# Optimization experiments

Measured on AMD Instinct MI355X. Metric: run time of the kernel, lower is better.

## Reference

```python
import jax, jax.numpy as jnp
import numpy as np

SPATIAL_SHAPES = [(128, 128), (64, 64), (32, 32), (16, 16)]
D_MODEL = 256
N_HEADS = 8
N_LEVELS = 4
N_POINTS = 4
HEAD_DIM = D_MODEL // N_HEADS
B = 2
LEN_Q = sum(h * w for h, w in SPATIAL_SHAPES)  # 21760
LEN_IN = LEN_Q


def setup_inputs() -> dict:
    key = jax.random.key(0)
    ks = jax.random.split(key, 11)
    s = 1.0 / np.sqrt(D_MODEL).astype(np.float32)
    query = jax.random.normal(ks[0], (B, LEN_Q, D_MODEL), jnp.float32)
    reference_points = jax.random.uniform(ks[1], (B, LEN_Q, N_LEVELS, 2), jnp.float32)
    input_flatten = jax.random.normal(ks[2], (B, LEN_IN, D_MODEL), jnp.float32)
    W_off = jax.random.normal(ks[3], (D_MODEL, N_HEADS * N_LEVELS * N_POINTS * 2), jnp.float32) * s
    b_off = jnp.zeros((N_HEADS * N_LEVELS * N_POINTS * 2,), jnp.float32)
    W_attn = jax.random.normal(ks[4], (D_MODEL, N_HEADS * N_LEVELS * N_POINTS), jnp.float32) * s
    b_attn = jnp.zeros((N_HEADS * N_LEVELS * N_POINTS,), jnp.float32)
    W_val = jax.random.normal(ks[5], (D_MODEL, D_MODEL), jnp.float32) * s
    b_val = jnp.zeros((D_MODEL,), jnp.float32)
    W_out = jax.random.normal(ks[6], (D_MODEL, D_MODEL), jnp.float32) * s
    b_out = jnp.zeros((D_MODEL,), jnp.float32)
    return {"query": query, "reference_points": reference_points, "input_flatten": input_flatten,
            "W_off": W_off, "b_off": b_off, "W_attn": W_attn, "b_attn": b_attn,
            "W_val": W_val, "b_val": b_val, "W_out": W_out, "b_out": b_out}


def _ms_deform_core(value, sampling_locations, attention_weights):
    # value: (B, H, Dh, N_total); sampling_locations: (B, Lq, H, L, P, 2) in [0,1]
    # attention_weights: (B, Lq, H, L*P)
    Bv, Hn, Dh, _ = value.shape
    Lq = sampling_locations.shape[1]
    P = sampling_locations.shape[4]
    BN = Bv * Hn
    grids = 2.0 * sampling_locations - 1.0
    splits = np.cumsum([h * w for h, w in SPATIAL_SHAPES])[:-1].tolist()
    value_list = jnp.split(value, splits, axis=3)
    sampled_levels = []
    for lid, (Hh, Ww) in enumerate(SPATIAL_SHAPES):
        # (BN, H*W, Dh)
        val_flat = jnp.transpose(value_list[lid].reshape(BN, Dh, Hh * Ww), (0, 2, 1))
        # (BN, Lq, P, 2)
        g = jnp.transpose(grids[:, :, :, lid, :, :], (0, 2, 1, 3, 4)).reshape(BN, Lq, P, 2)
        ix = ((g[..., 0] + 1.0) * Ww - 1.0) / 2.0
        iy = ((g[..., 1] + 1.0) * Hh - 1.0) / 2.0
        ix0 = jnp.floor(ix).astype(jnp.int32)
        iy0 = jnp.floor(iy).astype(jnp.int32)
        ix1 = ix0 + 1
        iy1 = iy0 + 1
        fx = (ix - ix0.astype(ix.dtype))[..., None]
        fy = (iy - iy0.astype(iy.dtype))[..., None]

        def valid(yy, xx):
            return ((xx >= 0) & (xx < Ww) & (yy >= 0) & (yy < Hh)).astype(val_flat.dtype)[..., None]

        def gather(yy, xx):
            idx = (jnp.clip(yy, 0, Hh - 1) * Ww + jnp.clip(xx, 0, Ww - 1)).reshape(BN, Lq * P)
            out = jnp.take_along_axis(val_flat, idx[:, :, None], axis=1)
            return out.reshape(BN, Lq, P, Dh)

        v00 = gather(iy0, ix0) * valid(iy0, ix0)
        v01 = gather(iy0, ix1) * valid(iy0, ix1)
        v10 = gather(iy1, ix0) * valid(iy1, ix0)
        v11 = gather(iy1, ix1) * valid(iy1, ix1)
        sampled = ((1 - fx) * (1 - fy) * v00 + fx * (1 - fy) * v01
                   + (1 - fx) * fy * v10 + fx * fy * v11)  # (BN, Lq, P, Dh)
        sampled_levels.append(jnp.transpose(sampled, (0, 3, 1, 2)))  # (BN, Dh, Lq, P)
    # (BN, Dh, Lq, L*P)
    sv = jnp.stack(sampled_levels, axis=-2).reshape(BN, Dh, Lq, N_LEVELS * P)
    attn = jnp.transpose(attention_weights, (0, 2, 1, 3)).reshape(BN, 1, Lq, N_LEVELS * P)
    out = jnp.sum(sv * attn, axis=-1)  # (BN, Dh, Lq)
    out = out.reshape(Bv, Hn * Dh, Lq)
    return jnp.transpose(out, (0, 2, 1))  # (B, Lq, d_model)


def reference(query, reference_points, input_flatten, W_off, b_off, W_attn, b_attn, W_val, b_val, W_out, b_out):
    Bq, Lq, _ = query.shape
    Len_in = input_flatten.shape[1]
    value = input_flatten @ W_val + b_val  # (B, Len_in, d_model)
    offsets = (query @ W_off + b_off).reshape(Bq, Lq, N_HEADS, N_LEVELS, N_POINTS, 2)
    attn = jax.nn.softmax((query @ W_attn + b_attn).reshape(Bq, Lq, N_HEADS, N_LEVELS * N_POINTS), axis=-1)
    # normalizer is (W, H) per level
    offset_normalizer = jnp.asarray([[w, h] for h, w in SPATIAL_SHAPES], dtype=query.dtype)
    sampling_locations = (reference_points[:, :, None, :, None, :]
                          + offsets / offset_normalizer[None, None, None, :, None, :])
    value = jnp.transpose(value, (0, 2, 1)).reshape(Bq, N_HEADS, HEAD_DIM, Len_in)
    out = _ms_deform_core(value, sampling_locations, attn)
    return out @ W_out + b_out
```

## Files before the change

### kernel.cpp

```cpp
#include <hip/hip_runtime.h>
#include <hip/hip_bf16.h>
#include <type_traits>

#define B_    2
#define LQ_   21760
#define LEN_  21760
#define DM    256
#define NH    8
#define NL    4
#define NP    4
#define HD    32

#define WS_VAL   0u
#define WS_QBF   22282240u
#define WS_INBF  44564480u
#define WS_OA    66846720u
#define WS_WT    133693440u

typedef __attribute__((ext_vector_type(4))) float f32x4;
typedef __attribute__((ext_vector_type(8))) short bf16x8;
typedef __attribute__((ext_vector_type(4))) unsigned int u32x4;

__device__ __forceinline__ unsigned short f2bf(float v) {
    __hip_bfloat16 h = __float2bfloat16(v);
    return *reinterpret_cast<unsigned short*>(&h);
}
__device__ __forceinline__ unsigned int pk2bf(float a, float b) {
    return (unsigned int)f2bf(a) | ((unsigned int)f2bf(b) << 16);
}

__global__ __launch_bounds__(256) void cvt_bf16(const float* __restrict__ x,
                                                unsigned short* __restrict__ y, int n4) {
    int i = blockIdx.x * 256 + threadIdx.x;
    if (i < n4) {
        f32x4 v = __builtin_nontemporal_load((const f32x4*)x + i);
        ushort4 u;
        u.x = f2bf(v.x); u.y = f2bf(v.y); u.z = f2bf(v.z); u.w = f2bf(v.w);
        ((ushort4*)y)[i] = u;
    }
}

__global__ __launch_bounds__(256) void wt_cvt(const float* __restrict__ W,
                                              unsigned short* __restrict__ Wt,
                                              int K, int N) {
    __shared__ float tile[16][17];
    const int n0 = blockIdx.x * 16, k0 = blockIdx.y * 16;
    const int tx = threadIdx.x & 15, ty = threadIdx.x >> 4;
    tile[ty][tx] = W[(size_t)(k0 + ty) * N + n0 + tx];
    __syncthreads();
    Wt[(size_t)(n0 + ty) * K + k0 + tx] = f2bf(tile[tx][ty]);
}

template <typename TOut>
__global__ __launch_bounds__(256) void gemm_mfma(const unsigned short* __restrict__ A,
                                                 const unsigned short* __restrict__ Bt,
                                                 const float* __restrict__ bias,
                                                 const float* __restrict__ bias2,
                                                 int nsplit,
                                                 TOut* __restrict__ C,
                                                 int M, int N, int K) {
    __shared__ unsigned short As[128 * 32];
    __shared__ unsigned short Bs[128 * 32];
    const int t = threadIdx.x;
    const int wv = t >> 6;
    const int ln = t & 63;
    const int m0 = blockIdx.x * 128;
    const int n0 = blockIdx.y * 128;
    const int wm = (wv & 1) * 64;
    const int wn = (wv >> 1) * 64;
    const int lrow = ln & 15;
    const int kq = ln >> 4;

    f32x4 acc[4][4] = {};

    for (int k0 = 0; k0 < K; k0 += 32) {
#pragma unroll
        for (int c = 0; c < 2; ++c) {
            const int o = c * 4096 + wv * 1024 + ln * 16;
            const int row = o >> 6;
            const int ke = (o & 63) >> 1;
            const unsigned short* ga = A + (size_t)(m0 + row) * K + k0 + ke;
            const unsigned short* gb = Bt + (size_t)(n0 + row) * K + k0 + ke;
            __builtin_amdgcn_global_load_lds(
                (const __attribute__((address_space(1))) void*)ga,
                (__attribute__((address_space(3))) void*)((char*)As + o), 16, 0, 0);
            __builtin_amdgcn_global_load_lds(
                (const __attribute__((address_space(1))) void*)gb,
                (__attribute__((address_space(3))) void*)((char*)Bs + o), 16, 0, 0);
        }
        __syncthreads();

        bf16x8 af[4], bfr[4];
#pragma unroll
        for (int i = 0; i < 4; ++i) {
            af[i]  = *(const bf16x8*)((char*)As + (wm + i * 16 + lrow) * 64 + kq * 16);
            bfr[i] = *(const bf16x8*)((char*)Bs + (wn + i * 16 + lrow) * 64 + kq * 16);
        }
#pragma unroll
        for (int i = 0; i < 4; ++i)
#pragma unroll
            for (int j = 0; j < 4; ++j)
                acc[i][j] = __builtin_amdgcn_mfma_f32_16x16x32_bf16(af[i], bfr[j], acc[i][j], 0, 0, 0);
        __syncthreads();
    }

#pragma unroll
    for (int j = 0; j < 4; ++j) {
        const int n = n0 + wn + j * 16 + lrow;
        const float bb = (n < nsplit) ? bias[n] : bias2[n - nsplit];
#pragma unroll
        for (int i = 0; i < 4; ++i) {
            const int mrow = m0 + wm + i * 16 + kq * 4;
#pragma unroll
            for (int r = 0; r < 4; ++r) {
                const float v = acc[i][j][r] + bb;
                if constexpr (std::is_same<TOut, float>::value) {
                    C[(size_t)(mrow + r) * N + n] = v;
                } else {
                    C[(size_t)(mrow + r) * N + n] = f2bf(v);
                }
            }
        }
    }
}

#define QB 8
__global__ __launch_bounds__(256) void msda_sample3(const unsigned short* __restrict__ value,
                                                    const float* __restrict__ oa,
                                                    const float* __restrict__ refp,
                                                    unsigned short* __restrict__ samp) {
    __shared__ char smem[16384 + 256];
    unsigned int* s_pk   = (unsigned int*)smem;
    float* s_off   = (float*)smem;
    float* s_logit = (float*)(smem + 8192);
    float* s_aw    = (float*)(smem + 12288);
    float* s_ref   = (float*)(smem + 16384);

    const int t = threadIdx.x;
    const int j = blockIdx.x;
    const int bq0 = ((j & 7) * 680 + (j >> 3)) * QB;
    const int b = bq0 / LQ_;

    {
        const float* oab = oa + (size_t)bq0 * 384;
#pragma unroll
        for (int r = 0; r < 2; ++r) {
            const int i = t + r * 256;
            const int ql = i >> 6, c = i & 63;
            ((f32x4*)s_off)[ql * 64 + c] =
                __builtin_nontemporal_load((const f32x4*)(oab + (size_t)ql * 384) + c);
        }
        {
            const int ql = t >> 5, c = t & 31;
            ((f32x4*)s_logit)[ql * 32 + c] =
                __builtin_nontemporal_load((const f32x4*)(oab + (size_t)ql * 384 + 256) + c);
        }
        if (t < 16)
            ((f32x4*)s_ref)[t] = __builtin_nontemporal_load((const f32x4*)(refp + (size_t)bq0 * 8) + t);
    }
    __syncthreads();

    if (t < 64) {
        const float* lg = s_logit + (t >> 3) * 128 + (t & 7) * 16;
        float m = -1e30f;
#pragma unroll
        for (int i = 0; i < 16; ++i) m = fmaxf(m, lg[i]);
        float e[16], s = 0.f;
#pragma unroll
        for (int i = 0; i < 16; ++i) { e[i] = __expf(lg[i] - m); s += e[i]; }
        const float inv = 1.f / s;
#pragma unroll
        for (int i = 0; i < 16; ++i) s_aw[t * 16 + i] = e[i] * inv;
    }
    __syncthreads();

    unsigned int pk0[4], pk1[4], pk2[4], pk3[4];
    {
        const int Wls[4] = {128, 64, 32, 16};
        const int Hls[4] = {128, 64, 32, 16};
        const int st_[4] = {0, 16384, 20480, 21504};
#pragma unroll
        for (int ii = 0; ii < 4; ++ii) {
            const int s = t * 4 + ii;
            const int q = s >> 7;
            const int rest = s & 127;
            const int h = rest >> 4;
            const int l = (rest >> 2) & 3;
            const int Wl = Wls[l], Hl = Hls[l], base = st_[l];
            const float ix = s_ref[q * 8 + l * 2]     * (float)Wl - 0.5f + s_off[q * 256 + rest * 2];
            const float iy = s_ref[q * 8 + l * 2 + 1] * (float)Hl - 0.5f + s_off[q * 256 + rest * 2 + 1];
            const float fix = floorf(ix), fiy = floorf(iy);
            const int x0 = (int)fix, y0 = (int)fiy;
            const int x1 = x0 + 1, y1 = y0 + 1;
            const float fx = ix - fix, fy = iy - fiy;
            const bool vx0 = (x0 >= 0) & (x0 < Wl);
            const bool vx1 = (x1 >= 0) & (x1 < Wl);
            const bool vy0 = (y0 >= 0) & (y0 < Hl);
            const bool vy1 = (y1 >= 0) & (y1 < Hl);
            const int cx0 = min(max(x0, 0), Wl - 1);
            const int cx1 = min(max(x1, 0), Wl - 1);
            const int cy0 = min(max(y0, 0), Hl - 1);
            const int cy1 = min(max(y1, 0), Hl - 1);
            const float aw = s_aw[(q * 8 + h) * 16 + (rest & 15)];
            const float w00 = aw * (1.f - fx) * (1.f - fy) * (float)(vx0 && vy0);
            const float w01 = aw * fx * (1.f - fy)         * (float)(vx1 && vy0);
            const float w10 = aw * (1.f - fx) * fy         * (float)(vx0 && vy1);
            const float w11 = aw * fx * fy                 * (float)(vx1 && vy1);
            pk0[ii] = (unsigned int)(base + cy0 * Wl + cx0) | ((unsigned int)(base + cy0 * Wl + cx1) << 16);
            pk1[ii] = (unsigned int)(base + cy1 * Wl + cx0) | ((unsigned int)(base + cy1 * Wl + cx1) << 16);
            pk2[ii] = pk2bf(w00, w01);
            pk3[ii] = pk2bf(w10, w11);
        }
    }
    __syncthreads();

#pragma unroll
    for (int ii = 0; ii < 4; ++ii) {
        const int s = t * 4 + ii;
        const int q = s >> 7;
        const int h = (s >> 4) & 7;
        const int swz = ((h & 3) << 2) ^ ((((h >> 2) ^ (q & 1)) & 1) << 4);
        *(uint4*)&s_pk[(s * 4) ^ swz] = make_uint4(pk0[ii], pk1[ii], pk2[ii], pk3[ii]);
    }
    __syncthreads();

    const int q = t >> 5;
    const int w = t & 31;
    const int h = w >> 2;
    const int dg = w & 3;
    const int swz = ((h & 3) << 2) ^ ((((h >> 2) ^ (q & 1)) & 1) << 4);
    const unsigned short* vbase = value + (size_t)b * LEN_ * DM + h * HD + dg * 8;

    float acc[8] = {0.f, 0.f, 0.f, 0.f, 0.f, 0.f, 0.f, 0.f};
    const int sbase = q * 128 + h * 16;
#pragma unroll
    for (int lp = 0; lp < 16; ++lp) {
        const uint4 pk = *(const uint4*)&s_pk[((sbase + lp) * 4) ^ swz];
        const uint4 v00 = *(const uint4*)(vbase + (size_t)(pk.x & 0xffffu) * DM);
        const uint4 v01 = *(const uint4*)(vbase + (size_t)(pk.x >> 16) * DM);
        const uint4 v10 = *(const uint4*)(vbase + (size_t)(pk.y & 0xffffu) * DM);
        const uint4 v11 = *(const uint4*)(vbase + (size_t)(pk.y >> 16) * DM);
        const float w00 = __uint_as_float(pk.z << 16);
        const float w01 = __uint_as_float(pk.z & 0xffff0000u);
        const float w10 = __uint_as_float(pk.w << 16);
        const float w11 = __uint_as_float(pk.w & 0xffff0000u);
#pragma unroll
        for (int c = 0; c < 4; ++c) {
            const unsigned int u00 = (&v00.x)[c], u01 = (&v01.x)[c];
            const unsigned int u10 = (&v10.x)[c], u11 = (&v11.x)[c];
            float a0 = acc[c * 2], a1 = acc[c * 2 + 1];
            a0 = fmaf(w00, __uint_as_float(u00 << 16), a0);
            a1 = fmaf(w00, __uint_as_float(u00 & 0xffff0000u), a1);
            a0 = fmaf(w01, __uint_as_float(u01 << 16), a0);
            a1 = fmaf(w01, __uint_as_float(u01 & 0xffff0000u), a1);
            a0 = fmaf(w10, __uint_as_float(u10 << 16), a0);
            a1 = fmaf(w10, __uint_as_float(u10 & 0xffff0000u), a1);
            a0 = fmaf(w11, __uint_as_float(u11 << 16), a0);
            a1 = fmaf(w11, __uint_as_float(u11 & 0xffff0000u), a1);
            acc[c * 2] = a0;
            acc[c * 2 + 1] = a1;
        }
    }
    u32x4 o;
    o.x = pk2bf(acc[0], acc[1]);
    o.y = pk2bf(acc[2], acc[3]);
    o.z = pk2bf(acc[4], acc[5]);
    o.w = pk2bf(acc[6], acc[7]);
    __builtin_nontemporal_store(o, (u32x4*)(samp + (size_t)(bq0 + q) * 256 + h * HD + dg * 8));
}

extern "C" void kernel_launch(void* const* d_in, const int* in_sizes, int n_in,
                              void* d_out, int out_size, void* d_ws, size_t ws_size,
                              hipStream_t stream) {
    const float* query  = (const float*)d_in[0];
    const float* refp   = (const float*)d_in[1];
    const float* inpf   = (const float*)d_in[2];
    const float* W_off  = (const float*)d_in[3];
    const float* b_off  = (const float*)d_in[4];
    const float* W_attn = (const float*)d_in[5];
    const float* b_attn = (const float*)d_in[6];
    const float* W_val  = (const float*)d_in[7];
    const float* b_val  = (const float*)d_in[8];
    const float* W_out  = (const float*)d_in[9];
    const float* b_out  = (const float*)d_in[10];
    float* out = (float*)d_out;

    char* ws = (char*)d_ws;
    unsigned short* val_bf  = (unsigned short*)(ws + WS_VAL);
    unsigned short* q_bf    = (unsigned short*)(ws + WS_QBF);
    unsigned short* in_bf   = (unsigned short*)(ws + WS_INBF);
    unsigned short* samp_bf = (unsigned short*)(ws + WS_INBF);
    float* oa = (float*)(ws + WS_OA);
    unsigned short* Wt_val = (unsigned short*)(ws + WS_WT);
    unsigned short* Wt_oa  = (unsigned short*)(ws + WS_WT + 131072);
    unsigned short* Wt_out = (unsigned short*)(ws + WS_WT + 327680);

    const int M = B_ * LQ_;
    const int n4 = M * DM / 4;

    cvt_bf16<<<dim3((n4 + 255) / 256), 256, 0, stream>>>(inpf, in_bf, n4);
    cvt_bf16<<<dim3((n4 + 255) / 256), 256, 0, stream>>>(query, q_bf, n4);
    wt_cvt<<<dim3(16, 16), 256, 0, stream>>>(W_val, Wt_val, 256, 256);
    wt_cvt<<<dim3(16, 16), 256, 0, stream>>>(W_off, Wt_oa, 256, 256);
    wt_cvt<<<dim3(8, 16), 256, 0, stream>>>(W_attn, Wt_oa + 256 * 256, 256, 128);
    wt_cvt<<<dim3(16, 16), 256, 0, stream>>>(W_out, Wt_out, 256, 256);

    gemm_mfma<unsigned short><<<dim3(M / 128, 2), 256, 0, stream>>>(
        in_bf, Wt_val, b_val, b_val, 256, val_bf, M, 256, 256);
    gemm_mfma<float><<<dim3(M / 128, 3), 256, 0, stream>>>(
        q_bf, Wt_oa, b_off, b_attn, 256, oa, M, 384, 256);

    msda_sample3<<<dim3(M / QB), 256, 0, stream>>>(val_bf, oa, refp, samp_bf);

    gemm_mfma<float><<<dim3(M / 128, 2), 256, 0, stream>>>(
        samp_bf, Wt_out, b_out, b_out, 256, out, M, 256, 256);
}
```

Baseline: 328.1 us.

## Fuse fp32-to-bf16 input conversion into GEMMs and store intermediates as fp16

Drops the standalone bf16 conversion kernels for query and input. The value and offset/attention GEMMs now read fp32 rows directly, convert them in registers and write bf16 into shared memory. The value and offset/logit intermediates are stored as fp16 instead of bf16/fp32 to cut the sampler's traffic. The four weight-transpose launches are merged into one, and the sampling loop is unrolled two points at a time with fp16 weights. In exchange the A-tile is staged through synchronous register loads rather than async global-to-LDS copies, and fp16 intermediates risk range or precision differences.

```diff
diff --git a/kernel.cpp b/kernel.cpp
--- a/kernel.cpp
+++ b/kernel.cpp
@@ -1,5 +1,6 @@
 #include <hip/hip_runtime.h>
 #include <hip/hip_bf16.h>
+#include <hip/hip_fp16.h>
 #include <type_traits>
 
 #define B_    2
@@ -12,14 +13,14 @@
 #define HD    32
 
 #define WS_VAL   0u
-#define WS_QBF   22282240u
-#define WS_INBF  44564480u
-#define WS_OA    66846720u
-#define WS_WT    133693440u
+#define WS_SAMP  22282240u
+#define WS_OA    44564480u
+#define WS_WT    77987840u
 
 typedef __attribute__((ext_vector_type(4))) float f32x4;
 typedef __attribute__((ext_vector_type(8))) short bf16x8;
 typedef __attribute__((ext_vector_type(4))) unsigned int u32x4;
+typedef __attribute__((ext_vector_type(2))) unsigned int u32x2;
 
 __device__ __forceinline__ unsigned short f2bf(float v) {
     __hip_bfloat16 h = __float2bfloat16(v);
@@ -28,31 +29,34 @@
 __device__ __forceinline__ unsigned int pk2bf(float a, float b) {
     return (unsigned int)f2bf(a) | ((unsigned int)f2bf(b) << 16);
 }
-
-__global__ __launch_bounds__(256) void cvt_bf16(const float* __restrict__ x,
-                                                unsigned short* __restrict__ y, int n4) {
-    int i = blockIdx.x * 256 + threadIdx.x;
-    if (i < n4) {
-        f32x4 v = __builtin_nontemporal_load((const f32x4*)x + i);
-        ushort4 u;
-        u.x = f2bf(v.x); u.y = f2bf(v.y); u.z = f2bf(v.z); u.w = f2bf(v.w);
-        ((ushort4*)y)[i] = u;
-    }
-}
-
-__global__ __launch_bounds__(256) void wt_cvt(const float* __restrict__ W,
-                                              unsigned short* __restrict__ Wt,
-                                              int K, int N) {
+__device__ __forceinline__ unsigned int pk2h(float a, float b) {
+    __half2 h = __floats2half2_rn(a, b);
+    union { __half2 h; unsigned int u; } c; c.h = h; return c.u;
+}
+__device__ __forceinline__ __half2 u2h2(unsigned int u) {
+    union { unsigned int u; __half2 h; } c; c.u = u; return c.h;
+}
+
+__global__ __launch_bounds__(256) void wt_cvt_all(const float* __restrict__ Wv,
+                                                  const float* __restrict__ Wo,
+                                                  const float* __restrict__ Wa,
+                                                  const float* __restrict__ Wu,
+                                                  unsigned short* __restrict__ wt) {
+    const float* Ws[4] = {Wv, Wo, Wa, Wu};
+    const int Ns[4] = {256, 256, 128, 256};
+    const unsigned int dof[4] = {0u, 65536u, 131072u, 163840u};
+    const int m = blockIdx.z;
+    const int n0 = blockIdx.x * 16, k0 = blockIdx.y * 16;
+    if (n0 >= Ns[m]) return;
     __shared__ float tile[16][17];
-    const int n0 = blockIdx.x * 16, k0 = blockIdx.y * 16;
     const int tx = threadIdx.x & 15, ty = threadIdx.x >> 4;
-    tile[ty][tx] = W[(size_t)(k0 + ty) * N + n0 + tx];
-    __syncthreads();
-    Wt[(size_t)(n0 + ty) * K + k0 + tx] = f2bf(tile[tx][ty]);
-}
-
-template <typename TOut>
-__global__ __launch_bounds__(256) void gemm_mfma(const unsigned short* __restrict__ A,
+    tile[ty][tx] = Ws[m][(size_t)(k0 + ty) * Ns[m] + n0 + tx];
+    __syncthreads();
+    wt[dof[m] + (size_t)(n0 + ty) * 256 + k0 + tx] = f2bf(tile[tx][ty]);
+}
+
+template <bool AF32, typename TOut>
+__global__ __launch_bounds__(256) void gemm_mfma(const void* __restrict__ Av,
                                                  const unsigned short* __restrict__ Bt,
                                                  const float* __restrict__ bias,
                                                  const float* __restrict__ bias2,
@@ -74,19 +78,43 @@
     f32x4 acc[4][4] = {};
 
     for (int k0 = 0; k0 < K; k0 += 32) {
-#pragma unroll
-        for (int c = 0; c < 2; ++c) {
-            const int o = c * 4096 + wv * 1024 + ln * 16;
-            const int row = o >> 6;
-            const int ke = (o & 63) >> 1;
-            const unsigned short* ga = A + (size_t)(m0 + row) * K + k0 + ke;
-            const unsigned short* gb = Bt + (size_t)(n0 + row) * K + k0 + ke;
-            __builtin_amdgcn_global_load_lds(
-                (const __attribute__((address_space(1))) void*)ga,
-                (__attribute__((address_space(3))) void*)((char*)As + o), 16, 0, 0);
-            __builtin_amdgcn_global_load_lds(
-                (const __attribute__((address_space(1))) void*)gb,
-                (__attribute__((address_space(3))) void*)((char*)Bs + o), 16, 0, 0);
+        if constexpr (AF32) {
+            const float* Af = (const float*)Av;
+#pragma unroll
+            for (int c = 0; c < 4; ++c) {
+                const int i = t + c * 256;
+                const int row = i >> 3;
+                const int kq4 = (i & 7) * 4;
+                f32x4 v = *(const f32x4*)&Af[(size_t)(m0 + row) * K + k0 + kq4];
+                uint2 p = make_uint2(pk2bf(v.x, v.y), pk2bf(v.z, v.w));
+                *(uint2*)((char*)As + row * 64 + kq4 * 2) = p;
+            }
+#pragma unroll
+            for (int c = 0; c < 2; ++c) {
+                const int o = c * 4096 + t * 16;
+                const int row = o >> 6;
+                const int ke = (o & 63) >> 1;
+                const unsigned short* gb = Bt + (size_t)(n0 + row) * K + k0 + ke;
+                __builtin_amdgcn_global_load_lds(
+                    (const __attribute__((address_space(1))) void*)gb,
+                    (__attribute__((address_space(3))) void*)((char*)Bs + o), 16, 0, 0);
+            }
+        } else {
+            const unsigned short* Ab = (const unsigned short*)Av;
+#pragma unroll
+            for (int c = 0; c < 2; ++c) {
+                const int o = c * 4096 + t * 16;
+                const int row = o >> 6;
+                const int ke = (o & 63) >> 1;
+                const unsigned short* ga = Ab + (size_t)(m0 + row) * K + k0 + ke;
+                const unsigned short* gb = Bt + (size_t)(n0 + row) * K + k0 + ke;
+                __builtin_amdgcn_global_load_lds(
+                    (const __attribute__((address_space(1))) void*)ga,
+                    (__attribute__((address_space(3))) void*)((char*)As + o), 16, 0, 0);
+                __builtin_amdgcn_global_load_lds(
+                    (const __attribute__((address_space(1))) void*)gb,
+                    (__attribute__((address_space(3))) void*)((char*)Bs + o), 16, 0, 0);
+            }
         }
         __syncthreads();
 
@@ -116,6 +144,8 @@
                 const float v = acc[i][j][r] + bb;
                 if constexpr (std::is_same<TOut, float>::value) {
                     C[(size_t)(mrow + r) * N + n] = v;
+                } else if constexpr (std::is_same<TOut, __half>::value) {
+                    C[(size_t)(mrow + r) * N + n] = __float2half(v);
                 } else {
                     C[(size_t)(mrow + r) * N + n] = f2bf(v);
                 }
@@ -125,12 +155,21 @@
 }
 
 #define QB 8
-__global__ __launch_bounds__(256) void msda_sample3(const unsigned short* __restrict__ value,
-                                                    const float* __restrict__ oa,
+__device__ __forceinline__ void accum4(const uint4& v, float w, float* acc) {
+#pragma unroll
+    for (int c = 0; c < 4; ++c) {
+        const __half2 h = u2h2((&v.x)[c]);
+        acc[c * 2]     = fmaf(w, __low2float(h),  acc[c * 2]);
+        acc[c * 2 + 1] = fmaf(w, __high2float(h), acc[c * 2 + 1]);
+    }
+}
+
+__global__ __launch_bounds__(256) void msda_sample4(const unsigned short* __restrict__ value,
+                                                    const unsigned short* __restrict__ oa,
                                                     const float* __restrict__ refp,
                                                     unsigned short* __restrict__ samp) {
     __shared__ char smem[16384 + 256];
-    unsigned int* s_pk   = (unsigned int*)smem;
+    unsigned int* s_pk = (unsigned int*)smem;
     float* s_off   = (float*)smem;
     float* s_logit = (float*)(smem + 8192);
     float* s_aw    = (float*)(smem + 12288);
@@ -142,18 +181,26 @@
     const int b = bq0 / LQ_;
 
     {
-        const float* oab = oa + (size_t)bq0 * 384;
-#pragma unroll
-        for (int r = 0; r < 2; ++r) {
-            const int i = t + r * 256;
-            const int ql = i >> 6, c = i & 63;
-            ((f32x4*)s_off)[ql * 64 + c] =
-                __builtin_nontemporal_load((const f32x4*)(oab + (size_t)ql * 384) + c);
-        }
+        const unsigned short* oab = oa + (size_t)bq0 * 384;
         {
             const int ql = t >> 5, c = t & 31;
-            ((f32x4*)s_logit)[ql * 32 + c] =
-                __builtin_nontemporal_load((const f32x4*)(oab + (size_t)ql * 384 + 256) + c);
+            u32x4 raw = __builtin_nontemporal_load((const u32x4*)(oab + (size_t)ql * 384) + c);
+            float2 f0 = __half22float2(u2h2(raw.x));
+            float2 f1 = __half22float2(u2h2(raw.y));
+            float2 f2 = __half22float2(u2h2(raw.z));
+            float2 f3 = __half22float2(u2h2(raw.w));
+            f32x4 o0 = {f0.x, f0.y, f1.x, f1.y};
+            f32x4 o1 = {f2.x, f2.y, f3.x, f3.y};
+            ((f32x4*)s_off)[ql * 64 + c * 2] = o0;
+            ((f32x4*)s_off)[ql * 64 + c * 2 + 1] = o1;
+        }
+        {
+            const int ql = t >> 5, c = t & 31;
+            u32x2 raw = __builtin_nontemporal_load((const u32x2*)(oab + (size_t)ql * 384 + 256) + c);
+            float2 f0 = __half22float2(u2h2(raw.x));
+            float2 f1 = __half22float2(u2h2(raw.y));
+            f32x4 o0 = {f0.x, f0.y, f1.x, f1.y};
+            ((f32x4*)s_logit)[ql * 32 + c] = o0;
         }
         if (t < 16)
             ((f32x4*)s_ref)[t] = __builtin_nontemporal_load((const f32x4*)(refp + (size_t)bq0 * 8) + t);
@@ -208,8 +255,8 @@
             const float w11 = aw * fx * fy                 * (float)(vx1 && vy1);
             pk0[ii] = (unsigned int)(base + cy0 * Wl + cx0) | ((unsigned int)(base + cy0 * Wl + cx1) << 16);
             pk1[ii] = (unsigned int)(base + cy1 * Wl + cx0) | ((unsigned int)(base + cy1 * Wl + cx1) << 16);
-            pk2[ii] = pk2bf(w00, w01);
-            pk3[ii] = pk2bf(w10, w11);
+            pk2[ii] = pk2h(w00, w01);
+            pk3[ii] = pk2h(w10, w11);
         }
     }
     __syncthreads();
@@ -234,32 +281,27 @@
     float acc[8] = {0.f, 0.f, 0.f, 0.f, 0.f, 0.f, 0.f, 0.f};
     const int sbase = q * 128 + h * 16;
 #pragma unroll
-    for (int lp = 0; lp < 16; ++lp) {
-        const uint4 pk = *(const uint4*)&s_pk[((sbase + lp) * 4) ^ swz];
-        const uint4 v00 = *(const uint4*)(vbase + (size_t)(pk.x & 0xffffu) * DM);
-        const uint4 v01 = *(const uint4*)(vbase + (size_t)(pk.x >> 16) * DM);
-        const uint4 v10 = *(const uint4*)(vbase + (size_t)(pk.y & 0xffffu) * DM);
-        const uint4 v11 = *(const uint4*)(vbase + (size_t)(pk.y >> 16) * DM);
-        const float w00 = __uint_as_float(pk.z << 16);
-        const float w01 = __uint_as_float(pk.z & 0xffff0000u);
-        const float w10 = __uint_as_float(pk.w << 16);
-        const float w11 = __uint_as_float(pk.w & 0xffff0000u);
-#pragma unroll
-        for (int c = 0; c < 4; ++c) {
-            const unsigned int u00 = (&v00.x)[c], u01 = (&v01.x)[c];
-            const unsigned int u10 = (&v10.x)[c], u11 = (&v11.x)[c];
-            float a0 = acc[c * 2], a1 = acc[c * 2 + 1];
-            a0 = fmaf(w00, __uint_as_float(u00 << 16), a0);
-            a1 = fmaf(w00, __uint_as_float(u00 & 0xffff0000u), a1);
-            a0 = fmaf(w01, __uint_as_float(u01 << 16), a0);
-            a1 = fmaf(w01, __uint_as_float(u01 & 0xffff0000u), a1);
-            a0 = fmaf(w10, __uint_as_float(u10 << 16), a0);
-            a1 = fmaf(w10, __uint_as_float(u10 & 0xffff0000u), a1);
-            a0 = fmaf(w11, __uint_as_float(u11 << 16), a0);
-            a1 = fmaf(w11, __uint_as_float(u11 & 0xffff0000u), a1);
-            acc[c * 2] = a0;
-            acc[c * 2 + 1] = a1;
-        }
+    for (int lp2 = 0; lp2 < 8; ++lp2) {
+        const uint4 pkA = *(const uint4*)&s_pk[((sbase + 2 * lp2)     * 4) ^ swz];
+        const uint4 pkB = *(const uint4*)&s_pk[((sbase + 2 * lp2 + 1) * 4) ^ swz];
+        const uint4 a00 = *(const uint4*)(vbase + (size_t)(pkA.x & 0xffffu) * DM);
+        const uint4 a01 = *(const uint4*)(vbase + (size_t)(pkA.x >> 16) * DM);
+        const uint4 a10 = *(const uint4*)(vbase + (size_t)(pkA.y & 0xffffu) * DM);
+        const uint4 a11 = *(const uint4*)(vbase + (size_t)(pkA.y >> 16) * DM);
+        const uint4 b00 = *(const uint4*)(vbase + (size_t)(pkB.x & 0xffffu) * DM);
+        const uint4 b01 = *(const uint4*)(vbase + (size_t)(pkB.x >> 16) * DM);
+        const uint4 b10 = *(const uint4*)(vbase + (size_t)(pkB.y & 0xffffu) * DM);
+        const uint4 b11 = *(const uint4*)(vbase + (size_t)(pkB.y >> 16) * DM);
+        const __half2 wA0 = u2h2(pkA.z), wA1 = u2h2(pkA.w);
+        const __half2 wB0 = u2h2(pkB.z), wB1 = u2h2(pkB.w);
+        accum4(a00, __low2float(wA0),  acc);
+        accum4(a01, __high2float(wA0), acc);
+        accum4(a10, __low2float(wA1),  acc);
+        accum4(a11, __high2float(wA1), acc);
+        accum4(b00, __low2float(wB0),  acc);
+        accum4(b01, __high2float(wB0), acc);
+        accum4(b10, __low2float(wB1),  acc);
+        accum4(b11, __high2float(wB1), acc);
     }
     u32x4 o;
     o.x = pk2bf(acc[0], acc[1]);
@@ -286,32 +328,25 @@
     float* out = (float*)d_out;
 
     char* ws = (char*)d_ws;
-    unsigned short* val_bf  = (unsigned short*)(ws + WS_VAL);
-    unsigned short* q_bf    = (unsigned short*)(ws + WS_QBF);
-    unsigned short* in_bf   = (unsigned short*)(ws + WS_INBF);
-    unsigned short* samp_bf = (unsigned short*)(ws + WS_INBF);
-    float* oa = (float*)(ws + WS_OA);
-    unsigned short* Wt_val = (unsigned short*)(ws + WS_WT);
-    unsigned short* Wt_oa  = (unsigned short*)(ws + WS_WT + 131072);
-    unsigned short* Wt_out = (unsigned short*)(ws + WS_WT + 327680);
+    unsigned short* val_h  = (unsigned short*)(ws + WS_VAL);
+    unsigned short* samp_bf = (unsigned short*)(ws + WS_SAMP);
+    unsigned short* oa_h   = (unsigned short*)(ws + WS_OA);
+    unsigned short* wt     = (unsigned short*)(ws + WS_WT);
+    unsigned short* Wt_val = wt;
+    unsigned short* Wt_oa  = wt + 65536;
+    unsigned short* Wt_out = wt + 163840;
 
     const int M = B_ * LQ_;
-    const int n4 = M * DM / 4;
-
-    cvt_bf16<<<dim3((n4 + 255) / 256), 256, 0, stream>>>(inpf, in_bf, n4);
-    cvt_bf16<<<dim3((n4 + 255) / 256), 256, 0, stream>>>(query, q_bf, n4);
-    wt_cvt<<<dim3(16, 16), 256, 0, stream>>>(W_val, Wt_val, 256, 256);
-    wt_cvt<<<dim3(16, 16), 256, 0, stream>>>(W_off, Wt_oa, 256, 256);
-    wt_cvt<<<dim3(8, 16), 256, 0, stream>>>(W_attn, Wt_oa + 256 * 256, 256, 128);
-    wt_cvt<<<dim3(16, 16), 256, 0, stream>>>(W_out, Wt_out, 256, 256);
-
-    gemm_mfma<unsigned short><<<dim3(M / 128, 2), 256, 0, stream>>>(
-        in_bf, Wt_val, b_val, b_val, 256, val_bf, M, 256, 256);
-    gemm_mfma<float><<<dim3(M / 128, 3), 256, 0, stream>>>(
-        q_bf, Wt_oa, b_off, b_attn, 256, oa, M, 384, 256);
-
-    msda_sample3<<<dim3(M / QB), 256, 0, stream>>>(val_bf, oa, refp, samp_bf);
-
-    gemm_mfma<float><<<dim3(M / 128, 2), 256, 0, stream>>>(
+
+    wt_cvt_all<<<dim3(16, 16, 4), 256, 0, stream>>>(W_val, W_off, W_attn, W_out, wt);
+
+    gemm_mfma<true, __half><<<dim3(M / 128, 2), 256, 0, stream>>>(
+        inpf, Wt_val, b_val, b_val, 256, (__half*)val_h, M, 256, 256);
+    gemm_mfma<true, __half><<<dim3(M / 128, 3), 256, 0, stream>>>(
+        query, Wt_oa, b_off, b_attn, 256, (__half*)oa_h, M, 384, 256);
+
+    msda_sample4<<<dim3(M / QB), 256, 0, stream>>>(val_h, oa_h, refp, samp_bf);
+
+    gemm_mfma<false, float><<<dim3(M / 128, 2), 256, 0, stream>>>(
         samp_bf, Wt_out, b_out, b_out, 256, out, M, 256, 256);
 }
```

Result: faster. 296.5 us (-9.6%).
